# Optimization experiments

Hardware: AMD Instinct MI355X
Metric: run time of the kernel (lower is better)

Reference implementation:

```python
import jax, jax.numpy as jnp
import numpy as np

BSZ, SEQ, DK = 16, 2048, 64


def setup_inputs() -> dict:
    key = jax.random.key(0)
    kq, kk, kv, kp = jax.random.split(key, 4)
    Q = jax.random.normal(kq, (BSZ, SEQ, DK), dtype=jnp.float32)
    K = jax.random.normal(kk, (BSZ, SEQ, DK), dtype=jnp.float32)
    V = jax.random.normal(kv, (BSZ, SEQ, DK), dtype=jnp.float32)
    # learned relative-position key projection, Parameter(dk, sizeSeq)
    Krelpos = jax.random.normal(kp, (DK, SEQ), dtype=jnp.float32) * (1.0 / np.sqrt(DK))
    return {"Q": Q, "K": K, "V": V, "Krelpos": Krelpos}


def reference(Q, K, V, Krelpos):
    b, S, dk = Q.shape
    # content scores: [b, S, S]
    QK = jnp.einsum('bsd,btd->bst', Q, K)
    # relative-position bias via skew trick
    QP = jnp.einsum('bsd,dt->bst', Q, Krelpos)                     # [b, S, S]
    QP = jnp.concatenate([jnp.zeros((b, S, 1), QP.dtype), QP], axis=2)  # [b, S, S+1]
    QK = QK + QP.reshape(b, S + 1, S)[:, 1:, :]                    # skewed -> [b, S, S]
    # causal mask: -inf strictly above diagonal
    causal = jnp.tril(jnp.ones((S, S), dtype=bool))
    mask = jnp.where(causal, jnp.zeros((), QK.dtype), -jnp.inf)
    A = jax.nn.softmax(QK / jnp.sqrt(jnp.asarray(dk, QK.dtype)) + mask, axis=2)
    # dropout p=0.0 -> identity
    return jnp.einsum('bst,btd->bsd', A, V)
```

## Files before the change

### kernel.cpp

```cpp
#include <hip/hip_runtime.h>
#include <math.h>

#define BSZ 16
#define SEQ 2048
#define DKD 64
#define NTH 256

typedef __attribute__((ext_vector_type(8))) short bf16x8;
typedef __attribute__((ext_vector_type(8))) short short8;
typedef __attribute__((ext_vector_type(4))) float f32x4;

__device__ __forceinline__ short f2bf(float x) {
  union { float f; unsigned u; } c; c.f = x;
  unsigned r = c.u + 0x7fffu + ((c.u >> 16) & 1u);
  return (short)(r >> 16);
}

__device__ __forceinline__ int pkbf(float hi, float lo) {
  return (int)__builtin_amdgcn_perm(__float_as_uint(hi), __float_as_uint(lo), 0x07060302u);
}

#define GLD16(gsrc, ldst)                                                                  \
  __builtin_amdgcn_global_load_lds((const __attribute__((address_space(1))) void*)(gsrc), \
                                   (__attribute__((address_space(3))) void*)(ldst), 16, 0, 0)

#define CH(row, c8) (((row) << 3) + ((c8) ^ ((row) & 7)))


__launch_bounds__(NTH)
__global__ void pre_convert(const float* __restrict__ K, const float* __restrict__ V,
                            const float* __restrict__ P, short* __restrict__ Kbf,
                            short* __restrict__ VTbf, short* __restrict__ PTbf,
                            float* __restrict__ Ozero, float* __restrict__ Lzero) {
  __shared__ short T[64 * 65];
  const int blk = blockIdx.x;
  const int tid = threadIdx.x;
  if (blk < 1024) {
    const int b = blk >> 6, ch = blk & 63;
    const float* Kb = K + ((size_t)(b * SEQ + ch * 32)) * DKD;
    const float* Vb = V + ((size_t)(b * SEQ + ch * 32)) * DKD;
    const int r = tid >> 3, c8 = (tid & 7) << 3;
    float4 a0 = *(const float4*)(Kb + r * DKD + c8);
    float4 a1 = *(const float4*)(Kb + r * DKD + c8 + 4);
    short8 ko;
    ko[0] = f2bf(a0.x); ko[1] = f2bf(a0.y); ko[2] = f2bf(a0.z); ko[3] = f2bf(a0.w);
    ko[4] = f2bf(a1.x); ko[5] = f2bf(a1.y); ko[6] = f2bf(a1.z); ko[7] = f2bf(a1.w);
    *(short8*)(Kbf + ((size_t)(b * SEQ + ch * 32 + r)) * DKD + c8) = ko;
    float4 v0 = *(const float4*)(Vb + r * DKD + c8);
    float4 v1 = *(const float4*)(Vb + r * DKD + c8 + 4);
    T[(c8 + 0) * 33 + r] = f2bf(v0.x); T[(c8 + 1) * 33 + r] = f2bf(v0.y);
    T[(c8 + 2) * 33 + r] = f2bf(v0.z); T[(c8 + 3) * 33 + r] = f2bf(v0.w);
    T[(c8 + 4) * 33 + r] = f2bf(v1.x); T[(c8 + 5) * 33 + r] = f2bf(v1.y);
    T[(c8 + 6) * 33 + r] = f2bf(v1.z); T[(c8 + 7) * 33 + r] = f2bf(v1.w);
    __syncthreads();
    const int d = tid >> 2, qg = tid & 3;
    short8 w;
    #pragma unroll
    for (int j = 0; j < 4; ++j) {
      w[j]     = T[d * 33 + qg * 4 + j];
      w[4 + j] = T[d * 33 + 16 + qg * 4 + j];
    }
    *(short8*)(VTbf + ((size_t)(b * DKD + d)) * SEQ + ch * 32 + qg * 8) = w;
  } else if (blk < 1056) {
    const int c0 = (blk - 1024) * 64;
    const int d = tid >> 2, cc4 = (tid & 3) << 4;
    #pragma unroll
    for (int j4 = 0; j4 < 4; ++j4) {
      const int c = cc4 + j4 * 4;
      float4 pv = *(const float4*)(P + (size_t)d * SEQ + c0 + c);
      T[(c + 0) * 65 + d] = f2bf(pv.x);
      T[(c + 1) * 65 + d] = f2bf(pv.y);
      T[(c + 2) * 65 + d] = f2bf(pv.z);
      T[(c + 3) * 65 + d] = f2bf(pv.w);
    }
    __syncthreads();
    const int c = tid >> 2, d4 = (tid & 3) << 4;
    short8 w0, w1;
    #pragma unroll
    for (int j = 0; j < 8; ++j) { w0[j] = T[c * 65 + d4 + j]; w1[j] = T[c * 65 + d4 + 8 + j]; }
    short* Po = PTbf + ((size_t)(c0 + c)) * DKD + d4;
    *(short8*)(Po + 0) = w0;
    *(short8*)(Po + 8) = w1;
  } else if (blk == 1056) {
    short8 z = {0, 0, 0, 0, 0, 0, 0, 0};
    short* Po = PTbf + (size_t)SEQ * DKD + tid * 16;
    *(short8*)(Po + 0) = z;
    *(short8*)(Po + 8) = z;
  } else if (blk < 1569) {
    const int u = blk - 1057;
    float4 z = {0.f, 0.f, 0.f, 0.f};
    float4* p = (float4*)(Ozero + (size_t)u * 4096 + tid * 16);
    p[0] = z; p[1] = z; p[2] = z; p[3] = z;
  } else {
    const int u = blk - 1569;
    float4 z = {0.f, 0.f, 0.f, 0.f};
    float4* p = (float4*)(Lzero + (size_t)u * 4096 + tid * 16);
    p[0] = z; p[1] = z; p[2] = z; p[3] = z;
  }
}

__launch_bounds__(NTH, 5)
__global__ void attn_split(const float* __restrict__ Q,
                           const short* __restrict__ Kbf,
                           const short* __restrict__ VTbf,
                           const short* __restrict__ PTbf,
                           float* __restrict__ Oacc,
                           float* __restrict__ Lacc) {
  __shared__ __align__(16) short smem[16384];
  short* Ks  = smem;
  short* VsT = smem + 4096;
  short* PsT = smem + 8192;

  const int tid = threadIdx.x;
  const int lane = tid & 63;
  const int wave = tid >> 6;
  const int l16 = lane & 15;
  const int quad = lane >> 4;

  const int i = blockIdx.x;
  const int x = i & 7;
  const int t = i >> 3;
  const int b = x + 8 * (t & 1);
  const int h = (t >> 1) & 3;
  const int qidx = t >> 3;
  const int qt = (qidx < 16) ? (31 - qidx) : (qidx - 16);
  const int r0 = qt * 64;
  const int kt0 = ((qt + 1) * h) >> 2;
  const int kt1 = ((qt + 1) * (h + 1)) >> 2;
  const float SC = 0.125f * 1.4426950408889634f;

  bf16x8 aq[2];
  {
    const float* Qr = Q + ((size_t)(b * SEQ + r0 + wave * 16 + l16)) * DKD + quad * 8;
    #pragma unroll
    for (int ks = 0; ks < 2; ++ks) {
      float4 xq = *(const float4*)(Qr + ks * 32);
      float4 yq = *(const float4*)(Qr + ks * 32 + 4);
      bf16x8 tq;
      tq[0] = f2bf(xq.x * SC); tq[1] = f2bf(xq.y * SC); tq[2] = f2bf(xq.z * SC); tq[3] = f2bf(xq.w * SC);
      tq[4] = f2bf(yq.x * SC); tq[5] = f2bf(yq.y * SC); tq[6] = f2bf(yq.z * SC); tq[7] = f2bf(yq.w * SC);
      aq[ks] = tq;
    }
  }

  int gsrc[4];
  bool gcar[4];
  #pragma unroll
  for (int r = 0; r < 4; ++r) {
    int o = 15 - (quad * 4 + r);
    int ss = l16 + o;
    gsrc[r] = (quad << 4) | (ss & 15);
    gcar[r] = (ss >= 16);
  }

  union i4v { int4 i; bf16x8 v; };
  i4v ONESu; ONESu.i = make_int4(0x3F803F80, 0x3F803F80, 0x3F803F80, 0x3F803F80);
  i4v S0u, S1u;
  S0u.i = make_int4(0, 0, 0, 0);
  S1u.i = make_int4(0, 0, 0, 0);
  if (quad == (l16 >> 2)) {
    const int j = l16 & 3;
    const int val = 0x3F80 << ((j & 1) * 16);
    if (j < 2) { S0u.i.x = val; S1u.i.z = val; }
    else       { S0u.i.y = val; S1u.i.w = val; }
  }

  f32x4 oacc[4];
  #pragma unroll
  for (int tt = 0; tt < 4; ++tt)
    #pragma unroll
    for (int j = 0; j < 4; ++j) oacc[tt][j] = 0.f;
  f32x4 bl;
  #pragma unroll
  for (int j = 0; j < 4; ++j) bl[j] = 0.f;

  const int Blo0 = 31 - qt;

  for (int kt = kt0; kt < kt1; ++kt) {
    const int j0 = kt * 64;
    __syncthreads();

    #pragma unroll
    for (int half = 0; half < 2; ++half) {
      const int ii = wave * 2 + half;
      const int j = ii * 64 + lane;
      {
        const int k = j >> 3, c8 = (j & 7) ^ (k & 7);
        GLD16(Kbf + ((size_t)(b * SEQ + j0 + k)) * DKD + c8 * 8, Ks + ii * 512);
      }
      {
        const int d = j >> 3, c8 = (j & 7) ^ (d & 7);
        GLD16(VTbf + ((size_t)(b * DKD + d)) * SEQ + j0 + c8 * 8, VsT + ii * 512);
      }
    }
    {
      const int Bg = Blo0 + kt + 1;
      #pragma unroll
      for (int half = 0; half < 2; ++half) {
        const int ii = wave * 2 + half;
        const int j = ii * 64 + lane;
        const int c = j >> 3, c8 = (j & 7) ^ (c & 7);
        GLD16(PTbf + ((size_t)(Bg * 64 + c)) * DKD + c8 * 8,
              PsT + ((Bg & 1) << 12) + ii * 512);
      }
      if (kt == kt0) {
        const int Bl = Blo0 + kt0;
        #pragma unroll
        for (int half = 0; half < 2; ++half) {
          const int ii = wave * 2 + half;
          const int j = ii * 64 + lane;
          const int c = j >> 3, c8 = (j & 7) ^ (c & 7);
          GLD16(PTbf + ((size_t)(Bl * 64 + c)) * DKD + c8 * 8,
                PsT + ((Bl & 1) << 12) + ii * 512);
        }
      }
    }
    __syncthreads();

    f32x4 sacc[4];
    #pragma unroll
    for (int tt = 0; tt < 4; ++tt)
      #pragma unroll
      for (int j = 0; j < 4; ++j) sacc[tt][j] = 0.f;
    #pragma unroll
    for (int ks = 0; ks < 2; ++ks)
      #pragma unroll
      for (int tt = 0; tt < 4; ++tt) {
        bf16x8 bk = *(const bf16x8*)&Ks[CH(tt * 16 + l16, ks * 4 + quad) << 3];
        sacc[tt] = __builtin_amdgcn_mfma_f32_16x16x32_bf16(aq[ks], bk, sacc[tt], 0, 0, 0);
      }

    float g[5][4];
    #pragma unroll
    for (int tt = 0; tt < 5; ++tt) {
      f32x4 bacc;
      #pragma unroll
      for (int j = 0; j < 4; ++j) bacc[j] = 0.f;
      const int c = (tt + 3 - wave) * 16 + l16;
      const int pan = (Blo0 + kt + (c >> 6)) & 1;
      const int pr = c & 63;
      #pragma unroll
      for (int ks = 0; ks < 2; ++ks) {
        bf16x8 bp = *(const bf16x8*)&PsT[(pan << 12) + (CH(pr, ks * 4 + quad) << 3)];
        bacc = __builtin_amdgcn_mfma_f32_16x16x32_bf16(aq[ks], bp, bacc, 0, 0, 0);
      }
      #pragma unroll
      for (int r = 0; r < 4; ++r) g[tt][r] = __shfl(bacc[r], gsrc[r], 64);
    }

    const bool diag = (kt == qt);
    float e[4][4];
    #pragma unroll
    for (int tt = 0; tt < 4; ++tt)
      #pragma unroll
      for (int r = 0; r < 4; ++r) {
        float sc = sacc[tt][r] + (gcar[r] ? g[tt + 1][r] : g[tt][r]);
        if (diag && (tt * 16 + l16 > wave * 16 + quad * 4 + r)) sc = -INFINITY;
        e[tt][r] = exp2f(sc);
      }

    i4v ap0, ap1;
    ap0.i.x = pkbf(e[0][1], e[0][0]); ap0.i.y = pkbf(e[0][3], e[0][2]);
    ap0.i.z = pkbf(e[1][1], e[1][0]); ap0.i.w = pkbf(e[1][3], e[1][2]);
    ap1.i.x = pkbf(e[2][1], e[2][0]); ap1.i.y = pkbf(e[2][3], e[2][2]);
    ap1.i.z = pkbf(e[3][1], e[3][0]); ap1.i.w = pkbf(e[3][3], e[3][2]);

    f32x4 zero4;
    #pragma unroll
    for (int j = 0; j < 4; ++j) zero4[j] = 0.f;
    f32x4 Dt[4];
    Dt[0] = __builtin_amdgcn_mfma_f32_16x16x32_bf16(ap0.v, S0u.v, zero4, 0, 0, 0);
    Dt[1] = __builtin_amdgcn_mfma_f32_16x16x32_bf16(ap0.v, S1u.v, zero4, 0, 0, 0);
    Dt[2] = __builtin_amdgcn_mfma_f32_16x16x32_bf16(ap1.v, S0u.v, zero4, 0, 0, 0);
    Dt[3] = __builtin_amdgcn_mfma_f32_16x16x32_bf16(ap1.v, S1u.v, zero4, 0, 0, 0);

    i4v bp0, bp1;
    bp0.i.x = pkbf(Dt[0][1], Dt[0][0]); bp0.i.y = pkbf(Dt[0][3], Dt[0][2]);
    bp0.i.z = pkbf(Dt[1][1], Dt[1][0]); bp0.i.w = pkbf(Dt[1][3], Dt[1][2]);
    bp1.i.x = pkbf(Dt[2][1], Dt[2][0]); bp1.i.y = pkbf(Dt[2][3], Dt[2][2]);
    bp1.i.z = pkbf(Dt[3][1], Dt[3][0]); bp1.i.w = pkbf(Dt[3][3], Dt[3][2]);

    #pragma unroll
    for (int tp = 0; tp < 2; ++tp) {
      const bf16x8 bpk = tp ? bp1.v : bp0.v;
      bl = __builtin_amdgcn_mfma_f32_16x16x32_bf16(ONESu.v, bpk, bl, 0, 0, 0);
      #pragma unroll
      for (int dt = 0; dt < 4; ++dt) {
        bf16x8 av = *(const bf16x8*)&VsT[CH(dt * 16 + l16, tp * 4 + quad) << 3];
        oacc[dt] = __builtin_amdgcn_mfma_f32_16x16x32_bf16(av, bpk, oacc[dt], 0, 0, 0);
      }
    }
  }

  __syncthreads();
  float* Te = (float*)smem;
  #pragma unroll
  for (int dt = 0; dt < 4; ++dt)
    #pragma unroll
    for (int r = 0; r < 4; ++r)
      Te[(wave * 16 + l16) * 65 + dt * 16 + quad * 4 + r] = oacc[dt][r];
  __syncthreads();
  if (kt1 > kt0) {
    float* Ob = Oacc + ((size_t)(b * SEQ + r0)) * DKD;
    #pragma unroll
    for (int j = 0; j < 16; ++j) {
      const int idx = j * NTH + tid;
      const int row = idx >> 6, col = idx & 63;
      unsafeAtomicAdd(&Ob[(size_t)row * DKD + col], Te[row * 65 + col]);
    }
    if (quad == 0)
      unsafeAtomicAdd(&Lacc[b * SEQ + r0 + wave * 16 + l16], bl[0]);
  }
}

__launch_bounds__(NTH)
__global__ void norm_out(float* __restrict__ O, const float* __restrict__ L) {
  const int tid = threadIdx.x;
  const int row = blockIdx.x * 16 + (tid >> 4);
  const int c4 = (tid & 15) << 2;
  const float rl = 1.0f / L[row];
  float4* p = (float4*)(O + (size_t)row * DKD + c4);
  float4 v = *p;
  v.x *= rl; v.y *= rl; v.z *= rl; v.w *= rl;
  *p = v;
}

extern "C" void kernel_launch(void* const* d_in, const int* in_sizes, int n_in,
                              void* d_out, int out_size, void* d_ws, size_t ws_size,
                              hipStream_t stream) {
  const float* Q = (const float*)d_in[0];
  const float* K = (const float*)d_in[1];
  const float* V = (const float*)d_in[2];
  const float* P = (const float*)d_in[3];
  float* O = (float*)d_out;

  short* Kbf = (short*)d_ws;
  short* VTbf = (short*)((char*)d_ws + 4194304);
  short* PTbf = (short*)((char*)d_ws + 8388608);
  float* Lacc = (float*)((char*)d_ws + 8658944);

  hipLaunchKernelGGL(pre_convert, dim3(1577), dim3(NTH), 0, stream,
                     K, V, P, Kbf, VTbf, PTbf, O, Lacc);
  hipLaunchKernelGGL(attn_split, dim3(2048), dim3(NTH), 0, stream,
                     Q, Kbf, VTbf, PTbf, O, Lacc);
  hipLaunchKernelGGL(norm_out, dim3(BSZ * SEQ / 16), dim3(NTH), 0, stream, O, Lacc);
}
```

Before: 154.2 us.

## Reuse overlapping relpos bias tile across key tiles and remap block order

Each key tile's positional-bias computation overlaps the previous tile by one 16-column block, so the last bias block is carried in registers and reused as the first block of the next iteration. This drops two MFMAs and a shuffle per iteration after the first. The block-index mapping also changes so consecutive blocks share a query tile and iterate over batch and split, which alters cache locality and scheduling order. The cost is a branch and a few extra live registers.

```diff
diff --git a/kernel.cpp b/kernel.cpp
--- a/kernel.cpp
+++ b/kernel.cpp
@@ -118,11 +118,10 @@
   const int quad = lane >> 4;
 
   const int i = blockIdx.x;
-  const int x = i & 7;
-  const int t = i >> 3;
-  const int b = x + 8 * (t & 1);
-  const int h = (t >> 1) & 3;
-  const int qidx = t >> 3;
+  const int qidx = i >> 6;
+  const int s = i & 63;
+  const int b = s >> 2;
+  const int h = s & 3;
   const int qt = (qidx < 16) ? (31 - qidx) : (qidx - 16);
   const int r0 = qt * 64;
   const int kt0 = ((qt + 1) * h) >> 2;
@@ -176,6 +175,8 @@
 
   const int Blo0 = 31 - qt;
 
+  float g0c[4];
+
   for (int kt = kt0; kt < kt1; ++kt) {
     const int j0 = kt * 64;
     __syncthreads();
@@ -231,8 +232,26 @@
       }
 
     float g[5][4];
-    #pragma unroll
-    for (int tt = 0; tt < 5; ++tt) {
+    if (kt == kt0) {
+      f32x4 bacc;
+      #pragma unroll
+      for (int j = 0; j < 4; ++j) bacc[j] = 0.f;
+      const int c = (3 - wave) * 16 + l16;
+      const int pan = (Blo0 + kt + (c >> 6)) & 1;
+      const int pr = c & 63;
+      #pragma unroll
+      for (int ks = 0; ks < 2; ++ks) {
+        bf16x8 bp = *(const bf16x8*)&PsT[(pan << 12) + (CH(pr, ks * 4 + quad) << 3)];
+        bacc = __builtin_amdgcn_mfma_f32_16x16x32_bf16(aq[ks], bp, bacc, 0, 0, 0);
+      }
+      #pragma unroll
+      for (int r = 0; r < 4; ++r) g[0][r] = __shfl(bacc[r], gsrc[r], 64);
+    } else {
+      #pragma unroll
+      for (int r = 0; r < 4; ++r) g[0][r] = g0c[r];
+    }
+    #pragma unroll
+    for (int tt = 1; tt < 5; ++tt) {
       f32x4 bacc;
       #pragma unroll
       for (int j = 0; j < 4; ++j) bacc[j] = 0.f;
@@ -247,6 +266,8 @@
       #pragma unroll
       for (int r = 0; r < 4; ++r) g[tt][r] = __shfl(bacc[r], gsrc[r], 64);
     }
+    #pragma unroll
+    for (int r = 0; r < 4; ++r) g0c[r] = g[4][r];
 
     const bool diag = (kt == qt);
     float e[4][4];
```

Measured after the change: 152.8 us. No clear change (-0.9%).
